# Optimization experiments

Measured on AMD Instinct MI355X. Metric: run time of the kernel, lower is better.

Reference implementation:

```python
import jax, jax.numpy as jnp
import numpy as np
from jax import lax

PLENS = [2, 3, 4, 5, 6, 7]
NPAT = 50  # patterns per length
V, WD, T, H, C = 100000, 300, 2048, 100, 2
D = sum(p * 2 * NPAT for p in PLENS)  # 2700 diag rows actually used


def setup_inputs() -> dict:
    key = jax.random.key(0)
    ks = jax.random.split(key, 20)
    inp = {}
    inp['doc'] = jax.random.randint(ks[0], (T,), 0, V)
    inp['embeddings'] = jax.random.normal(ks[1], (V, WD), jnp.float32)
    diags = jax.random.normal(ks[2], (D, WD), jnp.float32)
    diags = diags / jnp.linalg.norm(diags, axis=1, keepdims=True)  # normalize() in __init__
    inp['diags'] = diags
    inp['bias'] = jax.random.normal(ks[3], (D,), jnp.float32)
    for i, p in enumerate(PLENS):
        inp[f'eps{p}'] = jax.random.normal(ks[4 + i], (NPAT, p - 1), jnp.float32)
    inp['epsilon_scale'] = 0.5 * jnp.ones((1,), jnp.float32)
    inp['self_loop_scale'] = 0.5 * jnp.ones((1,), jnp.float32)
    tot = NPAT * len(PLENS)  # 300
    inp['w1'] = jax.random.normal(ks[10], (tot, H), jnp.float32) * 0.05
    inp['b1'] = jax.random.normal(ks[11], (H,), jnp.float32) * 0.05
    inp['w2'] = jax.random.normal(ks[12], (H, C), jnp.float32) * 0.05
    inp['b2'] = jax.random.normal(ks[13], (C,), jnp.float32) * 0.05
    return inp


def _run_group(tm, eps, sls, plen):
    # tm: [T, NPAT, 2, plen]; eps: [NPAT, plen-1]; sls: [1] (self-loop scale)
    # sum-times semiring: zero=0, one=1, plus=add, times=mul
    one_col = jnp.ones((NPAT, 1), tm.dtype)
    zero_col = jnp.zeros((NPAT, 1), tm.dtype)
    h0 = jnp.concatenate([one_col, jnp.zeros((NPAT, plen - 1), tm.dtype)], axis=1)

    def step(carry, tm_t):
        h, sc = carry
        # epsilon transitions
        h = h + jnp.concatenate([zero_col, h[:, :-1] * eps], axis=1)
        # main (word) transitions with restart padding (semiring one)
        res = jnp.concatenate([one_col, h[:, :-1] * tm_t[:, 1, :-1]], axis=1)
        # scaled self-loops
        res = res + sls * (h * tm_t[:, 0, :])
        return (res, sc + res[:, -1]), None

    (_, sc), _ = lax.scan(step, (h0, jnp.zeros((NPAT,), tm.dtype)), tm)
    return sc  # [NPAT]


def reference(doc, embeddings, diags, bias, eps2, eps3, eps4, eps5, eps6, eps7,
              epsilon_scale, self_loop_scale, w1, b1, w2, b2):
    # all per-token transition values at once: [T, D]
    tm_full = jax.nn.sigmoid(embeddings[doc] @ diags.T + bias)
    sls = jax.nn.sigmoid(self_loop_scale)
    eps_sc = jax.nn.sigmoid(epsilon_scale)
    eps_list = [eps2, eps3, eps4, eps5, eps6, eps7]
    scores = []
    start = 0
    for p, eps_raw in zip(PLENS, eps_list):
        end = start + p * 2 * NPAT
        tm = tm_full[:, start:end].reshape(-1, NPAT, 2, p)
        eps = eps_sc * jax.nn.sigmoid(eps_raw)
        scores.append(_run_group(tm, eps, sls, p))
        start = end
    s = jnp.concatenate(scores)[None, :]  # [1, total_num_patterns]
    h = jax.nn.relu(s @ w1 + b1)
    return h @ w2 + b2  # logits [1, num_classes]
```

## Files before the change

kernel.cpp:

```cpp
#include <hip/hip_runtime.h>
#include <math.h>

#define T_LEN 2048
#define WD 300
#define DTOT 2700
#define NPAT 50
#define H_DIM 100
#define NCLS 2
#define CCH 64
#define SCH 32
#define TOTPAT 300
#define RSTRIDE 68
#define KP 320
#define ASTR 40

typedef short bf16x8 __attribute__((ext_vector_type(8)));
typedef float f32x4 __attribute__((ext_vector_type(4)));

__device__ __forceinline__ float sigm(float x) { return 1.f / (1.f + __expf(-x)); }

__device__ __forceinline__ unsigned short f2bf(float x) {
    unsigned int u = __float_as_uint(x);
    u += 0x7fffu + ((u >> 16) & 1u);
    return (unsigned short)(u >> 16);
}
__device__ __forceinline__ float bf2f(unsigned short h) {
    return __uint_as_float(((unsigned int)h) << 16);
}

#define NA2 (T_LEN * (KP / 2))
#define NB2 (DTOT * (KP / 2))

__global__ __launch_bounds__(256) void prepack(const int* __restrict__ doc,
                                               const float* __restrict__ emb,
                                               const float* __restrict__ diags,
                                               unsigned short* __restrict__ Ah,
                                               unsigned short* __restrict__ Al,
                                               unsigned short* __restrict__ Bh,
                                               unsigned short* __restrict__ Bl) {
    int gid = blockIdx.x * 256 + threadIdx.x;
    float2 v = make_float2(0.f, 0.f);
    unsigned short* ph;
    unsigned short* pl;
    size_t off;
    if (gid < NA2) {
        int t = gid / (KP / 2);
        int kk = (gid - t * (KP / 2)) * 2;
        if (kk < WD) v = *(const float2*)(emb + (size_t)doc[t] * WD + kk);
        off = (size_t)t * KP + kk;
        ph = Ah; pl = Al;
    } else {
        int b = gid - NA2;
        if (b >= NB2) return;
        int n = b / (KP / 2);
        int kk = (b - n * (KP / 2)) * 2;
        if (kk < WD) v = *(const float2*)(diags + (size_t)n * WD + kk);
        off = (size_t)n * KP + kk;
        ph = Bh; pl = Bl;
    }
    unsigned short h0 = f2bf(v.x), h1 = f2bf(v.y);
    unsigned short l0 = f2bf(v.x - bf2f(h0)), l1 = f2bf(v.y - bf2f(h1));
    ushort2 hv; hv.x = h0; hv.y = h1;
    ushort2 lv; lv.x = l0; lv.y = l1;
    *(ushort2*)(ph + off) = hv;
    *(ushort2*)(pl + off) = lv;
}

__global__ __launch_bounds__(256) void gemm_mfma(const unsigned short* __restrict__ Ah,
                                                 const unsigned short* __restrict__ Al,
                                                 const unsigned short* __restrict__ Bh,
                                                 const unsigned short* __restrict__ Bl,
                                                 const float* __restrict__ bias,
                                                 float* __restrict__ Cm) {
    __shared__ unsigned short sA[2][128][ASTR];
    __shared__ unsigned short sB[2][64][ASTR];
    int tid = threadIdx.x;
    int lane = tid & 63, wid = tid >> 6;
    int m0 = blockIdx.y * 128, n0 = blockIdx.x * 64;
    int wm = (wid >> 1) * 64;
    int wn = (wid & 1) * 32;

    f32x4 acc[4][2];
#pragma unroll
    for (int mi = 0; mi < 4; ++mi)
#pragma unroll
        for (int ni = 0; ni < 2; ++ni) acc[mi][ni] = (f32x4)(0.f);

    for (int k0 = 0; k0 < KP; k0 += 32) {
#pragma unroll
        for (int it = 0; it < 2; ++it) {
            int f = it * 256 + tid;
            int row = f >> 2, q = f & 3;
            size_t go = (size_t)(m0 + row) * KP + k0 + q * 8;
            *(uint4*)&sA[0][row][q * 8] = *(const uint4*)(Ah + go);
            *(uint4*)&sA[1][row][q * 8] = *(const uint4*)(Al + go);
        }
        {
            int row = tid >> 2, q = tid & 3;
            int nr = n0 + row; if (nr > DTOT - 1) nr = DTOT - 1;
            size_t go = (size_t)nr * KP + k0 + q * 8;
            *(uint4*)&sB[0][row][q * 8] = *(const uint4*)(Bh + go);
            *(uint4*)&sB[1][row][q * 8] = *(const uint4*)(Bl + go);
        }
        __syncthreads();

        int kc = (lane >> 4) * 8;
        int mr = lane & 15;
        bf16x8 ah[4], al[4], bh[2], bl[2];
#pragma unroll
        for (int mi = 0; mi < 4; ++mi) {
            ah[mi] = *(bf16x8*)&sA[0][wm + mi * 16 + mr][kc];
            al[mi] = *(bf16x8*)&sA[1][wm + mi * 16 + mr][kc];
        }
#pragma unroll
        for (int ni = 0; ni < 2; ++ni) {
            bh[ni] = *(bf16x8*)&sB[0][wn + ni * 16 + mr][kc];
            bl[ni] = *(bf16x8*)&sB[1][wn + ni * 16 + mr][kc];
        }
#pragma unroll
        for (int mi = 0; mi < 4; ++mi)
#pragma unroll
            for (int ni = 0; ni < 2; ++ni) {
                acc[mi][ni] = __builtin_amdgcn_mfma_f32_16x16x32_bf16(ah[mi], bh[ni], acc[mi][ni], 0, 0, 0);
                acc[mi][ni] = __builtin_amdgcn_mfma_f32_16x16x32_bf16(ah[mi], bl[ni], acc[mi][ni], 0, 0, 0);
                acc[mi][ni] = __builtin_amdgcn_mfma_f32_16x16x32_bf16(al[mi], bh[ni], acc[mi][ni], 0, 0, 0);
            }
        __syncthreads();
    }

    int mr = lane & 15;
    int rq = lane >> 4;
#pragma unroll
    for (int ni = 0; ni < 2; ++ni) {
        int col = n0 + wn + ni * 16 + mr;
        int cc = col < DTOT ? col : DTOT - 1;
        float bs = bias[cc];
        if (col < DTOT) {
#pragma unroll
            for (int mi = 0; mi < 4; ++mi)
#pragma unroll
                for (int r = 0; r < 4; ++r) {
                    int row = m0 + wm + mi * 16 + rq * 4 + r;
                    Cm[(size_t)row * DTOT + col] = sigm(acc[mi][ni][r] + bs);
                }
        }
    }
}

template <int P, int PBP>
__device__ void pass1_blk(int chunk, int patblk, const float* __restrict__ tm,
                          const float* __restrict__ epsr, float sls, float esc,
                          float* __restrict__ ws2, int g, float* __restrict__ sT,
                          int tid) {
    constexpr int NP1 = P + 1;
    constexpr int dstart = 100 * ((P * (P - 1)) / 2 - 1);
    constexpr int ROWF = PBP * 2 * P;
    constexpr int RB4 = ROWF / 4;
    constexpr int NF4 = SCH * RB4;

    const float* gbase = tm + (size_t)(chunk * SCH) * DTOT + dstart + patblk * ROWF;
#pragma unroll
    for (int i = 0; i < (NF4 + 63) / 64; ++i) {
        int f = i * 64 + tid;
        if (f < NF4) {
            int t = f / RB4;
            int q = f - t * RB4;
            *(float4*)&sT[t * ROWF + q * 4] = *(const float4*)(gbase + (size_t)t * DTOT + q * 4);
        }
    }
    __syncthreads();

    int patl = tid / NP1;
    int col = tid - patl * NP1;
    int pat = patblk * PBP + patl;
    if (patl < PBP && pat < NPAT) {
        float eps[P - 1];
#pragma unroll
        for (int j = 0; j < P - 1; ++j) eps[j] = esc * sigm(epsr[pat * (P - 1) + j]);

        float x[P];
#pragma unroll
        for (int i = 0; i < P; ++i) x[i] = 0.f;
        float inj = 0.f;
        if (col < P) x[col] = 1.f; else inj = 1.f;
        float qacc = 0.f;

        const float* lb = sT + patl * 2 * P;
#pragma unroll 4
        for (int t = 0; t < SCH; ++t) {
            float tv[2 * P];
            const float* row = lb + t * ROWF;
#pragma unroll
            for (int j = 0; j < P; ++j) {
                float2 u = *(const float2*)(row + 2 * j);
                tv[2 * j] = u.x;
                tv[2 * j + 1] = u.y;
            }
            float heps[P];
            heps[0] = x[0];
#pragma unroll
            for (int i = 1; i < P; ++i) heps[i] = fmaf(x[i - 1], eps[i - 1], x[i]);
            float res[P];
            res[0] = fmaf(heps[0], sls * tv[0], inj);
#pragma unroll
            for (int i = 1; i < P; ++i)
                res[i] = fmaf(heps[i - 1], tv[P + i - 1], heps[i] * (sls * tv[i]));
#pragma unroll
            for (int i = 0; i < P; ++i) x[i] = res[i];
            qacc += x[P - 1];
        }

        int gidx = g * NPAT + pat;
        float* dst = ws2 + ((size_t)(gidx * CCH + chunk)) * 64 + col * 8;
#pragma unroll
        for (int i = 0; i < P; ++i) dst[i] = x[i];
        dst[7] = qacc;
    }
}

__global__ __launch_bounds__(64) void pass1_kernel(const float* __restrict__ tm,
                                                   const float* __restrict__ e2,
                                                   const float* __restrict__ e3,
                                                   const float* __restrict__ e4,
                                                   const float* __restrict__ e5,
                                                   const float* __restrict__ e6,
                                                   const float* __restrict__ e7,
                                                   const float* __restrict__ eps_scale,
                                                   const float* __restrict__ sl_scale,
                                                   float* __restrict__ ws2) {
    __shared__ float sT[3584];
    int b = blockIdx.x;
    int chunk = b / 30;
    int r = b - chunk * 30;
    int tid = threadIdx.x;
    float sls = sigm(sl_scale[0]);
    float esc = sigm(eps_scale[0]);
    if (r < 3)       pass1_blk<2, 21>(chunk, r,      tm, e2, sls, esc, ws2, 0, sT, tid);
    else if (r < 7)  pass1_blk<3, 16>(chunk, r - 3,  tm, e3, sls, esc, ws2, 1, sT, tid);
    else if (r < 12) pass1_blk<4, 12>(chunk, r - 7,  tm, e4, sls, esc, ws2, 2, sT, tid);
    else if (r < 17) pass1_blk<5, 10>(chunk, r - 12, tm, e5, sls, esc, ws2, 3, sT, tid);
    else if (r < 23) pass1_blk<6, 9>(chunk, r - 17,  tm, e6, sls, esc, ws2, 4, sT, tid);
    else             pass1_blk<7, 8>(chunk, r - 23,  tm, e7, sls, esc, ws2, 5, sT, tid);
}

template <int P>
__device__ __forceinline__ void compose_rec(float* __restrict__ Arec,
                                            const float* __restrict__ Brec) {
    float MA[P][P], MB[P][P], vA[P], vB[P], qA[P], qB[P], rA, rB;
#pragma unroll
    for (int j = 0; j < P; ++j) {
#pragma unroll
        for (int i = 0; i < P; ++i) {
            MA[i][j] = Arec[j * 8 + i];
            MB[i][j] = Brec[j * 8 + i];
        }
        qA[j] = Arec[j * 8 + 7];
        qB[j] = Brec[j * 8 + 7];
    }
#pragma unroll
    for (int i = 0; i < P; ++i) {
        vA[i] = Arec[P * 8 + i];
        vB[i] = Brec[P * 8 + i];
    }
    rA = Arec[P * 8 + 7];
    rB = Brec[P * 8 + 7];

#pragma unroll
    for (int j = 0; j < P; ++j) {
        float mc[P];
#pragma unroll
        for (int i = 0; i < P; ++i) mc[i] = 0.f;
        float qc = qA[j];
#pragma unroll
        for (int k = 0; k < P; ++k) {
            float a = MA[k][j];
#pragma unroll
            for (int i = 0; i < P; ++i) mc[i] = fmaf(MB[i][k], a, mc[i]);
            qc = fmaf(qB[k], a, qc);
        }
#pragma unroll
        for (int i = 0; i < P; ++i) Arec[j * 8 + i] = mc[i];
        Arec[j * 8 + 7] = qc;
    }
    float vc[P];
#pragma unroll
    for (int i = 0; i < P; ++i) vc[i] = vB[i];
    float rc = rA + rB;
#pragma unroll
    for (int k = 0; k < P; ++k) {
        float a = vA[k];
#pragma unroll
        for (int i = 0; i < P; ++i) vc[i] = fmaf(MB[i][k], a, vc[i]);
        rc = fmaf(qB[k], a, rc);
    }
#pragma unroll
    for (int i = 0; i < P; ++i) Arec[P * 8 + i] = vc[i];
    Arec[P * 8 + 7] = rc;
}

template <int P>
__device__ void fold_pattern(const float* __restrict__ ws2, float* __restrict__ R,
                             float* __restrict__ scores, int gidx, int tid) {
    const float4* src = (const float4*)(ws2 + (size_t)gidx * CCH * 64);
#pragma unroll
    for (int j = 0; j < 16; ++j) {
        int f = j * 64 + tid;
        int rec = f >> 4;
        int q4 = f & 15;
        *(float4*)&R[rec * RSTRIDE + q4 * 4] = src[f];
    }
    for (int g = 1; g < CCH; g <<= 1) {
        __syncthreads();
        if ((tid & (2 * g - 1)) == 0)
            compose_rec<P>(&R[tid * RSTRIDE], &R[(tid + g) * RSTRIDE]);
    }
    __syncthreads();
    if (tid == 0) scores[gidx] = R[0 * 8 + 7] + R[P * 8 + 7];
}

__global__ __launch_bounds__(64) void pass2a_kernel(const float* __restrict__ ws2,
                                                    float* __restrict__ scores) {
    __shared__ float R[CCH * RSTRIDE];
    int gidx = blockIdx.x;
    int g = gidx / NPAT;
    int tid = threadIdx.x;
    switch (g) {
        case 0: fold_pattern<2>(ws2, R, scores, gidx, tid); break;
        case 1: fold_pattern<3>(ws2, R, scores, gidx, tid); break;
        case 2: fold_pattern<4>(ws2, R, scores, gidx, tid); break;
        case 3: fold_pattern<5>(ws2, R, scores, gidx, tid); break;
        case 4: fold_pattern<6>(ws2, R, scores, gidx, tid); break;
        case 5: fold_pattern<7>(ws2, R, scores, gidx, tid); break;
    }
}

__global__ __launch_bounds__(128) void mlp_kernel(const float* __restrict__ scores,
                                                  const float* __restrict__ w1,
                                                  const float* __restrict__ b1,
                                                  const float* __restrict__ w2,
                                                  const float* __restrict__ b2,
                                                  float* __restrict__ out) {
    __shared__ float s_lds[TOTPAT];
    __shared__ float h_lds[H_DIM];
    int tid = threadIdx.x;
    for (int i = tid; i < TOTPAT; i += 128) s_lds[i] = scores[i];
    __syncthreads();
    if (tid < H_DIM) {
        float a = b1[tid];
#pragma unroll 6
        for (int i = 0; i < TOTPAT; ++i) a = fmaf(s_lds[i], w1[i * H_DIM + tid], a);
        h_lds[tid] = fmaxf(a, 0.f);
    }
    __syncthreads();
    if (tid < NCLS) {
        float a = b2[tid];
        for (int j = 0; j < H_DIM; ++j) a = fmaf(h_lds[j], w2[j * NCLS + tid], a);
        out[tid] = a;
    }
}

extern "C" void kernel_launch(void* const* d_in, const int* in_sizes, int n_in,
                              void* d_out, int out_size, void* d_ws, size_t ws_size,
                              hipStream_t stream) {
    const int* doc = (const int*)d_in[0];
    const float* emb = (const float*)d_in[1];
    const float* diags = (const float*)d_in[2];
    const float* bias = (const float*)d_in[3];
    const float* e2 = (const float*)d_in[4];
    const float* e3 = (const float*)d_in[5];
    const float* e4 = (const float*)d_in[6];
    const float* e5 = (const float*)d_in[7];
    const float* e6 = (const float*)d_in[8];
    const float* e7 = (const float*)d_in[9];
    const float* eps_scale = (const float*)d_in[10];
    const float* sl_scale = (const float*)d_in[11];
    const float* w1 = (const float*)d_in[12];
    const float* b1 = (const float*)d_in[13];
    const float* w2 = (const float*)d_in[14];
    const float* b2 = (const float*)d_in[15];
    float* out = (float*)d_out;

    char* ws = (char*)d_ws;
    float* tm = (float*)ws;
    float* ws2 = (float*)(ws + 22118400);
    unsigned short* Ah = (unsigned short*)(ws + 22118400);
    unsigned short* Al = (unsigned short*)(ws + 23429120);
    unsigned short* Bh = (unsigned short*)(ws + 24739840);
    unsigned short* Bl = (unsigned short*)(ws + 26467840);
    float* scores = (float*)(ws + 28195840);

    hipLaunchKernelGGL(prepack, dim3((NA2 + NB2 + 255) / 256), dim3(256), 0, stream,
                       doc, emb, diags, Ah, Al, Bh, Bl);
    hipLaunchKernelGGL(gemm_mfma, dim3((DTOT + 63) / 64, T_LEN / 128), dim3(256), 0,
                       stream, Ah, Al, Bh, Bl, bias, tm);
    hipLaunchKernelGGL(pass1_kernel, dim3(CCH * 30), dim3(64), 0, stream,
                       tm, e2, e3, e4, e5, e6, e7, eps_scale, sl_scale, ws2);
    hipLaunchKernelGGL(pass2a_kernel, dim3(TOTPAT), dim3(64), 0, stream,
                       ws2, scores);
    hipLaunchKernelGGL(mlp_kernel, dim3(1), dim3(128), 0, stream,
                       scores, w1, b1, w2, b2, out);
}
```

Measured before the change: 248.9 us.

## Register-prefetch GEMM tiles and parallelize pass2 tree fold across columns

The GEMM main loop now loads the next K-slice of A/B hi/lo tiles into registers while MFMAs run on the current shared-memory tile, overlapping global latency with compute. The pass2 fold kernel grows to 256 threads and splits each record composition across P+1 threads, one per output column, instead of one thread per pair. This shortens the serial tree reduction. The cost is more barriers and more repeated shared-memory reads of the B record.

```diff
diff --git a/kernel.cpp b/kernel.cpp
--- a/kernel.cpp
+++ b/kernel.cpp
@@ -80,29 +80,44 @@
     int wm = (wid >> 1) * 64;
     int wn = (wid & 1) * 32;
 
+    int srow = tid >> 2, sq = tid & 3;
+    int nr = n0 + srow; if (nr > DTOT - 1) nr = DTOT - 1;
+    const size_t a0off = (size_t)(m0 + srow) * KP + sq * 8;
+    const size_t a1off = (size_t)(m0 + srow + 64) * KP + sq * 8;
+    const size_t boff = (size_t)nr * KP + sq * 8;
+
     f32x4 acc[4][2];
 #pragma unroll
     for (int mi = 0; mi < 4; ++mi)
 #pragma unroll
         for (int ni = 0; ni < 2; ++ni) acc[mi][ni] = (f32x4)(0.f);
 
+    uint4 pah0 = *(const uint4*)(Ah + a0off);
+    uint4 pah1 = *(const uint4*)(Ah + a1off);
+    uint4 pal0 = *(const uint4*)(Al + a0off);
+    uint4 pal1 = *(const uint4*)(Al + a1off);
+    uint4 pbh = *(const uint4*)(Bh + boff);
+    uint4 pbl = *(const uint4*)(Bl + boff);
+
     for (int k0 = 0; k0 < KP; k0 += 32) {
-#pragma unroll
-        for (int it = 0; it < 2; ++it) {
-            int f = it * 256 + tid;
-            int row = f >> 2, q = f & 3;
-            size_t go = (size_t)(m0 + row) * KP + k0 + q * 8;
-            *(uint4*)&sA[0][row][q * 8] = *(const uint4*)(Ah + go);
-            *(uint4*)&sA[1][row][q * 8] = *(const uint4*)(Al + go);
-        }
-        {
-            int row = tid >> 2, q = tid & 3;
-            int nr = n0 + row; if (nr > DTOT - 1) nr = DTOT - 1;
-            size_t go = (size_t)nr * KP + k0 + q * 8;
-            *(uint4*)&sB[0][row][q * 8] = *(const uint4*)(Bh + go);
-            *(uint4*)&sB[1][row][q * 8] = *(const uint4*)(Bl + go);
-        }
         __syncthreads();
+        *(uint4*)&sA[0][srow][sq * 8] = pah0;
+        *(uint4*)&sA[0][srow + 64][sq * 8] = pah1;
+        *(uint4*)&sA[1][srow][sq * 8] = pal0;
+        *(uint4*)&sA[1][srow + 64][sq * 8] = pal1;
+        *(uint4*)&sB[0][srow][sq * 8] = pbh;
+        *(uint4*)&sB[1][srow][sq * 8] = pbl;
+        __syncthreads();
+
+        if (k0 + 32 < KP) {
+            int kn = k0 + 32;
+            pah0 = *(const uint4*)(Ah + a0off + kn);
+            pah1 = *(const uint4*)(Ah + a1off + kn);
+            pal0 = *(const uint4*)(Al + a0off + kn);
+            pal1 = *(const uint4*)(Al + a1off + kn);
+            pbh = *(const uint4*)(Bh + boff + kn);
+            pbl = *(const uint4*)(Bl + boff + kn);
+        }
 
         int kc = (lane >> 4) * 8;
         int mr = lane & 15;
@@ -125,7 +140,6 @@
                 acc[mi][ni] = __builtin_amdgcn_mfma_f32_16x16x32_bf16(ah[mi], bl[ni], acc[mi][ni], 0, 0, 0);
                 acc[mi][ni] = __builtin_amdgcn_mfma_f32_16x16x32_bf16(al[mi], bh[ni], acc[mi][ni], 0, 0, 0);
             }
-        __syncthreads();
     }
 
     int mr = lane & 15;
@@ -244,82 +258,64 @@
 }
 
 template <int P>
-__device__ __forceinline__ void compose_rec(float* __restrict__ Arec,
-                                            const float* __restrict__ Brec) {
-    float MA[P][P], MB[P][P], vA[P], vB[P], qA[P], qB[P], rA, rB;
-#pragma unroll
-    for (int j = 0; j < P; ++j) {
-#pragma unroll
-        for (int i = 0; i < P; ++i) {
-            MA[i][j] = Arec[j * 8 + i];
-            MB[i][j] = Brec[j * 8 + i];
-        }
-        qA[j] = Arec[j * 8 + 7];
-        qB[j] = Brec[j * 8 + 7];
-    }
-#pragma unroll
-    for (int i = 0; i < P; ++i) {
-        vA[i] = Arec[P * 8 + i];
-        vB[i] = Brec[P * 8 + i];
-    }
-    rA = Arec[P * 8 + 7];
-    rB = Brec[P * 8 + 7];
-
-#pragma unroll
-    for (int j = 0; j < P; ++j) {
-        float mc[P];
-#pragma unroll
-        for (int i = 0; i < P; ++i) mc[i] = 0.f;
-        float qc = qA[j];
-#pragma unroll
-        for (int k = 0; k < P; ++k) {
-            float a = MA[k][j];
-#pragma unroll
-            for (int i = 0; i < P; ++i) mc[i] = fmaf(MB[i][k], a, mc[i]);
-            qc = fmaf(qB[k], a, qc);
-        }
-#pragma unroll
-        for (int i = 0; i < P; ++i) Arec[j * 8 + i] = mc[i];
-        Arec[j * 8 + 7] = qc;
-    }
-    float vc[P];
-#pragma unroll
-    for (int i = 0; i < P; ++i) vc[i] = vB[i];
-    float rc = rA + rB;
-#pragma unroll
-    for (int k = 0; k < P; ++k) {
-        float a = vA[k];
-#pragma unroll
-        for (int i = 0; i < P; ++i) vc[i] = fmaf(MB[i][k], a, vc[i]);
-        rc = fmaf(qB[k], a, rc);
-    }
-#pragma unroll
-    for (int i = 0; i < P; ++i) Arec[P * 8 + i] = vc[i];
-    Arec[P * 8 + 7] = rc;
-}
-
-template <int P>
 __device__ void fold_pattern(const float* __restrict__ ws2, float* __restrict__ R,
                              float* __restrict__ scores, int gidx, int tid) {
+    constexpr int NP1 = P + 1;
     const float4* src = (const float4*)(ws2 + (size_t)gidx * CCH * 64);
 #pragma unroll
-    for (int j = 0; j < 16; ++j) {
-        int f = j * 64 + tid;
+    for (int j = 0; j < 4; ++j) {
+        int f = j * 256 + tid;
         int rec = f >> 4;
         int q4 = f & 15;
         *(float4*)&R[rec * RSTRIDE + q4 * 4] = src[f];
     }
+    int pair = tid / NP1;
+    int col = tid - pair * NP1;
     for (int g = 1; g < CCH; g <<= 1) {
         __syncthreads();
-        if ((tid & (2 * g - 1)) == 0)
-            compose_rec<P>(&R[tid * RSTRIDE], &R[(tid + g) * RSTRIDE]);
+        int npairs = CCH / (2 * g);
+        if (pair < npairs) {
+            float* Ar = &R[(pair * 2 * g) * RSTRIDE];
+            const float* Br = &R[(pair * 2 * g + g) * RSTRIDE];
+            if (col < P) {
+                float MAj[P], mc[P];
+#pragma unroll
+                for (int i = 0; i < P; ++i) { MAj[i] = Ar[col * 8 + i]; mc[i] = 0.f; }
+                float qc = Ar[col * 8 + 7];
+#pragma unroll
+                for (int k = 0; k < P; ++k) {
+                    float a = MAj[k];
+#pragma unroll
+                    for (int i = 0; i < P; ++i) mc[i] = fmaf(Br[k * 8 + i], a, mc[i]);
+                    qc = fmaf(Br[k * 8 + 7], a, qc);
+                }
+#pragma unroll
+                for (int i = 0; i < P; ++i) Ar[col * 8 + i] = mc[i];
+                Ar[col * 8 + 7] = qc;
+            } else {
+                float vA[P], vc[P];
+#pragma unroll
+                for (int i = 0; i < P; ++i) { vA[i] = Ar[P * 8 + i]; vc[i] = Br[P * 8 + i]; }
+                float rc = Ar[P * 8 + 7] + Br[P * 8 + 7];
+#pragma unroll
+                for (int k = 0; k < P; ++k) {
+                    float a = vA[k];
+#pragma unroll
+                    for (int i = 0; i < P; ++i) vc[i] = fmaf(Br[k * 8 + i], a, vc[i]);
+                    rc = fmaf(Br[k * 8 + 7], a, rc);
+                }
+#pragma unroll
+                for (int i = 0; i < P; ++i) Ar[P * 8 + i] = vc[i];
+                Ar[P * 8 + 7] = rc;
+            }
+        }
     }
     __syncthreads();
     if (tid == 0) scores[gidx] = R[0 * 8 + 7] + R[P * 8 + 7];
 }
 
-__global__ __launch_bounds__(64) void pass2a_kernel(const float* __restrict__ ws2,
-                                                    float* __restrict__ scores) {
+__global__ __launch_bounds__(256) void pass2a_kernel(const float* __restrict__ ws2,
+                                                     float* __restrict__ scores) {
     __shared__ float R[CCH * RSTRIDE];
     int gidx = blockIdx.x;
     int g = gidx / NPAT;
@@ -395,7 +391,7 @@
                        stream, Ah, Al, Bh, Bl, bias, tm);
     hipLaunchKernelGGL(pass1_kernel, dim3(CCH * 30), dim3(64), 0, stream,
                        tm, e2, e3, e4, e5, e6, e7, eps_scale, sl_scale, ws2);
-    hipLaunchKernelGGL(pass2a_kernel, dim3(TOTPAT), dim3(64), 0, stream,
+    hipLaunchKernelGGL(pass2a_kernel, dim3(TOTPAT), dim3(256), 0, stream,
                        ws2, scores);
     hipLaunchKernelGGL(mlp_kernel, dim3(1), dim3(128), 0, stream,
                        scores, w1, b1, w2, b2, out);
```

Measured after the change: 244.3 us. No clear change (-1.8%).
